# Performance work log

Hardware: AMD Instinct MI355X
Metric: run time of the kernel (lower is better)

The kernel has to match this reference:

```python
import jax, jax.numpy as jnp
import numpy as np
import math

RIEMANN_ZEROS_IM = (14.134725142, 21.022039639, 25.01085758, 30.424876126, 32.935061588,
    37.586178159, 40.918719012, 43.327073281, 48.005150881, 49.773832478, 52.970321478,
    56.446247697, 59.347044003, 60.831778525, 65.112544048, 67.079810529, 69.546401711,
    72.067157674, 75.704690699, 77.144840069, 79.33737502, 82.910380854, 84.735492981,
    87.425274613, 88.809111208, 92.491899271, 94.651344041, 95.870634228, 98.831194218,
    101.317851006, 103.72553804, 105.446623052)

D_MODEL = 1024
N_HEADS = 16
D_HEAD = D_MODEL // N_HEADS  # 64
N_PAIRS = D_HEAD // 2        # 32

# normalized inverse frequencies: gamma_n / gamma_1, inverted
_gamma = np.asarray(RIEMANN_ZEROS_IM[:N_PAIRS], dtype=np.float32)
INV_FREQ = jnp.asarray(1.0 / (_gamma / _gamma[0]))  # [n_pairs]


def _rotate(x, cos, sin):
    # x: [b,h,n,d_head]; cos/sin: [1,h,n,n_pairs]; interleaved pair rotation
    x1 = x[..., 0::2]
    x2 = x[..., 1::2]
    rx1 = x1 * cos - x2 * sin
    rx2 = x1 * sin + x2 * cos
    return jnp.stack([rx1, rx2], axis=-1).reshape(x.shape)


def setup_inputs() -> dict:
    key = jax.random.key(0)
    k1, k2, k3 = jax.random.split(key, 3)
    b, n = 4, 2048
    x = jax.random.normal(k1, (b, n, D_MODEL), dtype=jnp.float32)
    # torch Linear(d, 3d, bias=False): y = x @ W.T; we store W.T directly
    w_qkv = jax.random.normal(k2, (D_MODEL, 3 * D_MODEL), dtype=jnp.float32) / math.sqrt(D_MODEL)
    w_o = jax.random.normal(k3, (D_MODEL, D_MODEL), dtype=jnp.float32) / math.sqrt(D_MODEL)
    log_scale = jnp.zeros((N_HEADS,), dtype=jnp.float32)
    return {"x": x, "w_qkv": w_qkv, "w_o": w_o, "log_scale": log_scale}


def reference(x, w_qkv, w_o, log_scale):
    b, n, d = x.shape
    qkv = (x @ w_qkv).reshape(b, n, 3, N_HEADS, D_HEAD)
    q, k, v = qkv[:, :, 0], qkv[:, :, 1], qkv[:, :, 2]  # [b,n,h,dh]
    q = q.transpose(0, 2, 1, 3)  # [b,h,n,dh]
    k = k.transpose(0, 2, 1, 3)
    v = v.transpose(0, 2, 1, 3)

    scale = jnp.exp(log_scale)  # [h]
    pos = jnp.arange(n, dtype=jnp.float32)
    # theta: [1,h,n,n_pairs]
    theta = pos[None, None, :, None] * INV_FREQ[None, None, None, :] * scale[None, :, None, None]
    cos, sin = jnp.cos(theta), jnp.sin(theta)
    q = _rotate(q, cos, sin)
    k = _rotate(k, cos, sin)

    scores = jnp.einsum('bhqd,bhkd->bhqk', q, k) / math.sqrt(D_HEAD)
    causal = jnp.tril(jnp.ones((n, n), dtype=bool))
    scores = jnp.where(causal[None, None], scores, -jnp.inf)
    attn = jax.nn.softmax(scores, axis=-1)
    out = jnp.einsum('bhqk,bhkd->bhqd', attn, v)
    out = out.transpose(0, 2, 1, 3).reshape(b, n, d)
    return out @ w_o
```

## Files before the change

kernel.cpp:

```cpp
#include <hip/hip_runtime.h>
#include <hip/hip_bf16.h>

#define B_ 4
#define N_ 2048
#define DM 1024
#define NH 16
#define DH 64

typedef __attribute__((ext_vector_type(8))) __bf16 bf16x8;
typedef __attribute__((ext_vector_type(4))) float f32x4;
typedef __attribute__((ext_vector_type(4))) float float4v;
typedef __attribute__((ext_vector_type(4))) unsigned int uint4v;
typedef __attribute__((ext_vector_type(2))) unsigned int uint2v;
typedef __attribute__((ext_vector_type(4))) unsigned short ushort4v;

__device__ __forceinline__ float bf2f(unsigned short h) {
  union { unsigned int u; float f; } v; v.u = ((unsigned int)h) << 16; return v.f;
}
__device__ __forceinline__ unsigned short f2bf(float f) {
  __bf16 h = (__bf16)f;
  return __builtin_bit_cast(unsigned short, h);
}
__device__ __forceinline__ f32x4 mfma16(bf16x8 a, bf16x8 b, f32x4 c) {
  return __builtin_amdgcn_mfma_f32_16x16x32_bf16(a, b, c, 0, 0, 0);
}
__device__ __forceinline__ void gload_lds16(const void* g, void* l) {
  __builtin_amdgcn_global_load_lds(
      (const __attribute__((address_space(1))) unsigned int*)g,
      (__attribute__((address_space(3))) unsigned int*)l, 16, 0, 0);
}
__device__ __forceinline__ float fexp2(float x) {
  return __builtin_amdgcn_exp2f(x);
}

__constant__ float GAMMA_C[32] = {
  14.134725142f, 21.022039639f, 25.01085758f, 30.424876126f,
  32.935061588f, 37.586178159f, 40.918719012f, 43.327073281f,
  48.005150881f, 49.773832478f, 52.970321478f, 56.446247697f,
  59.347044003f, 60.831778525f, 65.112544048f, 67.079810529f,
  69.546401711f, 72.067157674f, 75.704690699f, 77.144840069f,
  79.33737502f,  82.910380854f, 84.735492981f, 87.425274613f,
  88.809111208f, 92.491899271f, 94.651344041f, 95.870634228f,
  98.831194218f, 101.317851006f, 103.72553804f, 105.446623052f
};

__global__ __launch_bounds__(256) void cast_f32_bf16(
    const float* __restrict__ in, unsigned short* __restrict__ out, int n4) {
  int i = blockIdx.x * 256 + threadIdx.x;
  if (i >= n4) return;
  float4v v = *(const float4v*)&in[(size_t)i * 4];
  ushort4v o;
  o[0] = f2bf(v[0]); o[1] = f2bf(v[1]); o[2] = f2bf(v[2]); o[3] = f2bf(v[3]);
  *(ushort4v*)&out[(size_t)i * 4] = o;
}

__global__ __launch_bounds__(256) void tcast(
    const float* __restrict__ in, unsigned short* __restrict__ out, int K, int N) {
  __shared__ float t[32][33];
  int n0 = blockIdx.x * 32, k0 = blockIdx.y * 32;
  int tx = threadIdx.x, ty = threadIdx.y;
#pragma unroll
  for (int j = 0; j < 4; ++j)
    t[ty + j * 8][tx] = in[(size_t)(k0 + ty + j * 8) * N + n0 + tx];
  __syncthreads();
#pragma unroll
  for (int j = 0; j < 4; ++j)
    out[(size_t)(n0 + ty + j * 8) * K + k0 + tx] = f2bf(t[tx][ty + j * 8]);
}

template <int OUTF32>
__global__ __launch_bounds__(256) void gemm_bt(
    const unsigned short* __restrict__ A, const unsigned short* __restrict__ BT,
    void* __restrict__ C, int M, int N, int K) {
  __shared__ unsigned short As[128 * 32];
  __shared__ unsigned short Bs[128 * 32];
  int tid = threadIdx.x;
  int lane = tid & 63, wid = tid >> 6;
  int wr = wid >> 1, wc = wid & 1;
  int lr = lane & 15, lg = lane >> 4;
  int bm = blockIdx.y * 128, bn = blockIdx.x * 128;
  int srow = lane >> 2, sch = lane & 3;
  f32x4 acc[4][4];
#pragma unroll
  for (int m = 0; m < 4; ++m)
#pragma unroll
    for (int n = 0; n < 4; ++n) acc[m][n] = (f32x4){0.f, 0.f, 0.f, 0.f};

  for (int k0 = 0; k0 < K; k0 += 32) {
    __syncthreads();
#pragma unroll
    for (int it = 0; it < 2; ++it) {
      int rbase = wid * 16 + it * 64;
      gload_lds16(&A[(size_t)(bm + rbase + srow) * K + k0 + sch * 8],
                  &As[rbase * 32]);
      gload_lds16(&BT[(size_t)(bn + rbase + srow) * K + k0 + sch * 8],
                  &Bs[rbase * 32]);
    }
    __syncthreads();
    bf16x8 af[4], bfr[4];
#pragma unroll
    for (int m = 0; m < 4; ++m)
      af[m] = *(const bf16x8*)&As[(wr * 64 + m * 16 + lr) * 32 + lg * 8];
#pragma unroll
    for (int n = 0; n < 4; ++n)
      bfr[n] = *(const bf16x8*)&Bs[(wc * 64 + n * 16 + lr) * 32 + lg * 8];
    __builtin_amdgcn_s_setprio(1);
#pragma unroll
    for (int m = 0; m < 4; ++m)
#pragma unroll
      for (int n = 0; n < 4; ++n)
        acc[m][n] = mfma16(af[m], bfr[n], acc[m][n]);
    __builtin_amdgcn_s_setprio(0);
  }
#pragma unroll
  for (int m = 0; m < 4; ++m)
#pragma unroll
    for (int n = 0; n < 4; ++n) {
      int row = bm + wr * 64 + m * 16 + lg * 4;
      int col = bn + wc * 64 + n * 16 + lr;
#pragma unroll
      for (int r = 0; r < 4; ++r) {
        if (OUTF32)
          ((float*)C)[(size_t)(row + r) * N + col] = acc[m][n][r];
        else
          ((unsigned short*)C)[(size_t)(row + r) * N + col] = f2bf(acc[m][n][r]);
      }
    }
}

__global__ __launch_bounds__(256) void rope_split(
    const unsigned short* __restrict__ qkv, const float* __restrict__ log_scale,
    unsigned short* __restrict__ Qr, unsigned short* __restrict__ Kr) {
  const float SC = 0.125f * 1.44269504089f;
  int t = blockIdx.x * 256 + threadIdx.x;
  int p = t & 31, h = (t >> 5) & 15, n = (t >> 9) & 2047, b = t >> 20;
  float invf = GAMMA_C[0] / GAMMA_C[p];
  float scale = __expf(log_scale[h]);
  float theta = ((float)n * invf) * scale;
  float sn, cs;
  sincosf(theta, &sn, &cs);
  size_t base = (size_t)(b * N_ + n) * (3 * DM) + h * DH + 2 * p;
  unsigned int qu = *(const unsigned int*)&qkv[base];
  unsigned int ku = *(const unsigned int*)&qkv[base + DM];
  float q1 = bf2f(qu & 0xffffu), q2 = bf2f(qu >> 16);
  float k1 = bf2f(ku & 0xffffu), k2 = bf2f(ku >> 16);
  unsigned int rq = (unsigned int)f2bf((q1 * cs - q2 * sn) * SC) |
                    ((unsigned int)f2bf((q1 * sn + q2 * cs) * SC) << 16);
  unsigned int rk = (unsigned int)f2bf(k1 * cs - k2 * sn) |
                    ((unsigned int)f2bf(k1 * sn + k2 * cs) << 16);
  size_t ob = (size_t)((b * NH + h) * N_ + n) * DH + 2 * p;
  *(unsigned int*)&Qr[ob] = rq;
  *(unsigned int*)&Kr[ob] = rk;
}

__global__ __launch_bounds__(256) void attn_fwd(
    const unsigned short* __restrict__ Q, const unsigned short* __restrict__ K,
    const unsigned short* __restrict__ qkv, unsigned short* __restrict__ AO) {
  int orig = blockIdx.x;
  int wg = (orig & 7) * 128 + (orig >> 3);
  int i = wg & 15;
  int qt = ((wg >> 5) & 1) ? (15 - i) : i;
  int bh = wg >> 4;
  int b = bh >> 4, h = bh & 15;
  int q0 = qt * 128;
  int tid = threadIdx.x;
  int lane = tid & 63, w = tid >> 6;
  int lr = lane & 15, lg = lane >> 4;

  const unsigned short* Qh = Q + (size_t)bh * N_ * DH;
  const unsigned short* Kh = K + (size_t)bh * N_ * DH;
  const unsigned short* Vq = qkv + (size_t)b * N_ * (3 * DM) + 2 * DM + h * DH;

  __shared__ unsigned short Ks[2][64 * 64];
  __shared__ unsigned short Vt[64 * 64];
  __shared__ unsigned int PsU[4][32][32];

  bf16x8 qf[2][2];
#pragma unroll
  for (int m = 0; m < 2; ++m)
#pragma unroll
    for (int dh = 0; dh < 2; ++dh)
      qf[m][dh] = *(const bf16x8*)
          &Qh[(size_t)(q0 + w * 32 + m * 16 + lr) * DH + dh * 32 + lg * 8];

  f32x4 oacc[2][4];
#pragma unroll
  for (int m = 0; m < 2; ++m)
#pragma unroll
    for (int nb = 0; nb < 4; ++nb) oacc[m][nb] = (f32x4){0.f, 0.f, 0.f, 0.f};
  float mst[2] = {-1e30f, -1e30f};
  float lst[2] = {0.f, 0.f};

  int wkend = q0 + w * 32 + 31;
  int ksup = q0 + 128;
  int vch = tid & 7, vk = tid >> 3;
  int swz = 4 * (lr & 7);

  auto KSTAGE = [&](int buf, int kk0) {
#pragma unroll
    for (int it = 0; it < 2; ++it) {
      int rbase = w * 8 + it * 32;
      int row = rbase + (lane >> 3);
      int sk = ((row & 7) ^ (row >> 3)) & 7;
      int ch = lane & 7;
      gload_lds16(&Kh[(size_t)(kk0 + row) * DH + ((ch ^ sk) * 8)],
                  &Ks[buf][rbase * 64]);
    }
  };
  auto VWRITE = [&](uint4v v0, uint4v v1) {
    const unsigned short* p0 = (const unsigned short*)&v0;
    const unsigned short* p1 = (const unsigned short*)&v1;
#pragma unroll
    for (int j = 0; j < 8; ++j) {
      int d = vch * 8 + j;
      int sv = (j ^ vch) & 7;
      Vt[d * 64 + (vk ^ (sv << 3))] = p0[j];
      Vt[d * 64 + ((vk + 32) ^ (sv << 3))] = p1[j];
    }
  };

  {
    uint4v v0 = *(const uint4v*)&Vq[(size_t)vk * (3 * DM) + vch * 8];
    uint4v v1 = *(const uint4v*)&Vq[(size_t)(vk + 32) * (3 * DM) + vch * 8];
    KSTAGE(0, 0);
    VWRITE(v0, v1);
    __syncthreads();
  }
  int cur = 0;

  for (int k0 = 0; k0 < ksup; k0 += 64) {
    bool hn = (k0 + 64 < ksup);
    uint4v nv0, nv1;
    if (hn) {
      nv0 = *(const uint4v*)&Vq[(size_t)(k0 + 64 + vk) * (3 * DM) + vch * 8];
      nv1 = *(const uint4v*)&Vq[(size_t)(k0 + 96 + vk) * (3 * DM) + vch * 8];
      KSTAGE(cur ^ 1, k0 + 64);
    }

    if (k0 <= wkend) {
      f32x4 s[2][4];
      __builtin_amdgcn_s_setprio(1);
#pragma unroll
      for (int nb = 0; nb < 4; ++nb) {
        int key = nb * 16 + lr;
        int sk = ((key & 7) ^ (key >> 3)) & 7;
        bf16x8 kf0 = *(const bf16x8*)&Ks[cur][key * 64 + ((lg ^ sk) * 8)];
        bf16x8 kf1 = *(const bf16x8*)&Ks[cur][key * 64 + (((4 + lg) ^ sk) * 8)];
#pragma unroll
        for (int m = 0; m < 2; ++m) {
          f32x4 z = (f32x4){0.f, 0.f, 0.f, 0.f};
          z = mfma16(kf0, qf[m][0], z);
          z = mfma16(kf1, qf[m][1], z);
          s[m][nb] = z;
        }
      }
      __builtin_amdgcn_s_setprio(0);

      float mx[2];
#pragma unroll
      for (int m = 0; m < 2; ++m) {
        int qm = q0 + w * 32 + m * 16;
        if (k0 + 63 > qm) {
          int q = qm + lr;
#pragma unroll
          for (int nb = 0; nb < 4; ++nb)
#pragma unroll
            for (int r = 0; r < 4; ++r)
              if (k0 + nb * 16 + lg * 4 + r > q) s[m][nb][r] = -1e30f;
        }
        float mx0 = fmaxf(fmaxf(s[m][0][0], s[m][0][1]),
                          fmaxf(s[m][0][2], s[m][0][3]));
        float mx1 = fmaxf(fmaxf(s[m][1][0], s[m][1][1]),
                          fmaxf(s[m][1][2], s[m][1][3]));
        float mx2 = fmaxf(fmaxf(s[m][2][0], s[m][2][1]),
                          fmaxf(s[m][2][2], s[m][2][3]));
        float mx3 = fmaxf(fmaxf(s[m][3][0], s[m][3][1]),
                          fmaxf(s[m][3][2], s[m][3][3]));
        float m01 = fmaxf(fmaxf(mx0, mx1), fmaxf(mx2, mx3));
        m01 = fmaxf(m01, __shfl_xor(m01, 16, 64));
        m01 = fmaxf(m01, __shfl_xor(m01, 32, 64));
        mx[m] = m01;
      }

      if (__any((mx[0] > mst[0] + 8.f) || (mx[1] > mst[1] + 8.f))) {
        float scs[2];
#pragma unroll
        for (int m = 0; m < 2; ++m) {
          float mnew = fmaxf(mst[m], mx[m]);
          float sc = fexp2(mst[m] - mnew);
          mst[m] = mnew;
          lst[m] *= sc;
          scs[m] = sc;
        }
#pragma unroll
        for (int m = 0; m < 2; ++m)
#pragma unroll
          for (int r = 0; r < 4; ++r) {
            float scr = __shfl(scs[m], lg * 4 + r, 64);
#pragma unroll
            for (int nb = 0; nb < 4; ++nb) oacc[m][nb][r] *= scr;
          }
      }

#pragma unroll
      for (int m = 0; m < 2; ++m) {
        float ps = 0.f;
        unsigned int pw[8];
#pragma unroll
        for (int nb = 0; nb < 4; ++nb)
#pragma unroll
          for (int rp = 0; rp < 2; ++rp) {
            float p0 = fexp2(s[m][nb][2 * rp] - mst[m]);
            float p1 = fexp2(s[m][nb][2 * rp + 1] - mst[m]);
            ps += p0 + p1;
            pw[nb * 2 + rp] =
                (unsigned int)f2bf(p0) | ((unsigned int)f2bf(p1) << 16);
          }
#pragma unroll
        for (int nb = 0; nb < 4; ++nb) {
          int c0 = (nb * 8 + lg * 2) ^ swz;
          *(uint2v*)&PsU[w][m * 16 + lr][c0] =
              (uint2v){pw[nb * 2], pw[nb * 2 + 1]};
        }
        ps += __shfl_xor(ps, 16, 64);
        ps += __shfl_xor(ps, 32, 64);
        lst[m] += ps;
      }
      asm volatile("s_waitcnt lgkmcnt(0)" ::: "memory");
      __builtin_amdgcn_sched_barrier(0);

      __builtin_amdgcn_s_setprio(1);
#pragma unroll
      for (int kh = 0; kh < 2; ++kh) {
        bf16x8 pf0 = *(const bf16x8*)&PsU[w][lr][(kh * 16 + lg * 4) ^ swz];
        bf16x8 pf1 = *(const bf16x8*)&PsU[w][16 + lr][(kh * 16 + lg * 4) ^ swz];
#pragma unroll
        for (int nb = 0; nb < 4; ++nb) {
          int d = nb * 16 + lr;
          int sv2 = ((d & 7) ^ (d >> 3)) & 7;
          bf16x8 vf = *(const bf16x8*)
              &Vt[d * 64 + ((kh * 32 + lg * 8) ^ (sv2 << 3))];
          oacc[0][nb] = mfma16(pf0, vf, oacc[0][nb]);
          oacc[1][nb] = mfma16(pf1, vf, oacc[1][nb]);
        }
      }
      __builtin_amdgcn_s_setprio(0);
    }

    __syncthreads();
    if (hn) {
      VWRITE(nv0, nv1);
      __syncthreads();
    }
    cur ^= 1;
  }

#pragma unroll
  for (int m = 0; m < 2; ++m) {
    float inv = 1.0f / lst[m];
#pragma unroll
    for (int r = 0; r < 4; ++r) {
      float invr = __shfl(inv, lg * 4 + r, 64);
      int q = q0 + w * 32 + m * 16 + lg * 4 + r;
#pragma unroll
      for (int nb = 0; nb < 4; ++nb) {
        float o = oacc[m][nb][r] * invr;
        AO[(size_t)(b * N_ + q) * DM + h * DH + nb * 16 + lr] = f2bf(o);
      }
    }
  }
}

extern "C" void kernel_launch(void* const* d_in, const int* in_sizes, int n_in,
                              void* d_out, int out_size, void* d_ws, size_t ws_size,
                              hipStream_t stream) {
  const float* x = (const float*)d_in[0];
  const float* w_qkv = (const float*)d_in[1];
  const float* w_o = (const float*)d_in[2];
  const float* log_scale = (const float*)d_in[3];
  float* out = (float*)d_out;

  char* ws = (char*)d_ws;
  unsigned short* xb  = (unsigned short*)(ws);
  unsigned short* ao  = xb;
  unsigned short* wqT = (unsigned short*)(ws + (16u << 20));
  unsigned short* woT = (unsigned short*)(ws + (22u << 20));
  unsigned short* qkv = (unsigned short*)(ws + (24u << 20));
  unsigned short* Qr  = (unsigned short*)(ws + (72u << 20));
  unsigned short* Kr  = (unsigned short*)(ws + (88u << 20));

  cast_f32_bf16<<<8192, 256, 0, stream>>>(x, xb, (B_ * N_ * DM) / 4);
  dim3 tb(32, 8);
  tcast<<<dim3(3 * DM / 32, DM / 32), tb, 0, stream>>>(w_qkv, wqT, DM, 3 * DM);
  tcast<<<dim3(DM / 32, DM / 32), tb, 0, stream>>>(w_o, woT, DM, DM);
  gemm_bt<0><<<dim3(3 * DM / 128, (B_ * N_) / 128), 256, 0, stream>>>(
      xb, wqT, qkv, B_ * N_, 3 * DM, DM);
  rope_split<<<(B_ * N_ * NH * 32) / 256, 256, 0, stream>>>(
      qkv, log_scale, Qr, Kr);
  attn_fwd<<<B_ * NH * (N_ / 128), 256, 0, stream>>>(Qr, Kr, qkv, ao);
  gemm_bt<1><<<dim3(DM / 128, (B_ * N_) / 128), 256, 0, stream>>>(
      ao, woT, out, B_ * N_, DM, DM);
}
```

Before: 246.6 us.

## Use 256x128 eight-wave GEMM for QKV and pair causal attention tiles per block

Adds a new gemm256 kernel for the QKV projection. It uses 256x128 output tiles, 512 threads, double-buffered LDS staging through dynamic shared memory, and a barrier-split compute schedule, replacing the 128x128 gemm_bt for that projection. The attention kernel now processes two query tiles per block (tile pi and 15-pi), which balances causal work and halves the grid to 512 blocks. Risks are lower occupancy from the 96KB of LDS and fewer waves in flight for attention, plus the extra barriers in the GEMM loop.

```diff
diff --git a/kernel.cpp b/kernel.cpp
--- a/kernel.cpp
+++ b/kernel.cpp
@@ -125,6 +125,126 @@
         else
           ((unsigned short*)C)[(size_t)(row + r) * N + col] = f2bf(acc[m][n][r]);
       }
+    }
+}
+
+__global__ __launch_bounds__(512) void gemm256(
+    const unsigned short* __restrict__ A, const unsigned short* __restrict__ BT,
+    unsigned short* __restrict__ C, int M, int N, int K) {
+  extern __shared__ unsigned short smem[];
+  unsigned short* Asb = smem;
+  unsigned short* Bsb = smem + 32768;
+  int tid = threadIdx.x;
+  int lane = tid & 63, w = tid >> 6;
+  int wr = w >> 2, wc = w & 3;
+  int lr = lane & 15, lg = lane >> 4;
+  int nbx = N >> 7;
+  int cpx = gridDim.x >> 3;
+  int orig = blockIdx.x;
+  int wg = (orig & 7) * cpx + (orig >> 3);
+  int bm = (wg / nbx) << 8, bn = (wg % nbx) << 7;
+  int srow = lane >> 3, sch = lane & 7;
+
+  f32x4 acc[8][2];
+#pragma unroll
+  for (int m = 0; m < 8; ++m)
+#pragma unroll
+    for (int n = 0; n < 2; ++n) acc[m][n] = (f32x4){0.f, 0.f, 0.f, 0.f};
+
+  auto STAGE = [&](int buf, int t) {
+    int k0 = t << 6;
+#pragma unroll
+    for (int it = 0; it < 4; ++it) {
+      int rbase = w * 32 + it * 8;
+      int row = rbase + srow;
+      int sk = row & 7;
+      gload_lds16(&A[(size_t)(bm + row) * K + k0 + ((sch ^ sk) * 8)],
+                  &Asb[buf * 16384 + rbase * 64]);
+    }
+#pragma unroll
+    for (int it = 0; it < 2; ++it) {
+      int rbase = w * 16 + it * 8;
+      int row = rbase + srow;
+      int sk = row & 7;
+      gload_lds16(&BT[(size_t)(bn + row) * K + k0 + ((sch ^ sk) * 8)],
+                  &Bsb[buf * 8192 + rbase * 64]);
+    }
+  };
+
+  int NT = K >> 6;
+  STAGE(0, 0);
+  STAGE(1, 1);
+  asm volatile("s_waitcnt vmcnt(6)" ::: "memory");
+  __builtin_amdgcn_s_barrier();
+
+  bf16x8 a[4][2], b[2][2];
+  int cur = 0;
+  for (int t = 0; t < NT; ++t) {
+    const unsigned short* Ab = &Asb[cur * 16384];
+    const unsigned short* Bb = &Bsb[cur * 8192];
+
+#define RD_A(half)                                                         \
+  {                                                                        \
+    _Pragma("unroll") for (int m4 = 0; m4 < 4; ++m4) {                     \
+      int ra = wr * 128 + (half) * 64 + m4 * 16 + lr;                      \
+      _Pragma("unroll") for (int kk = 0; kk < 2; ++kk)                     \
+          a[m4][kk] = *(const bf16x8*)                                     \
+              &Ab[ra * 64 + (((kk * 4 + lg) ^ (ra & 7)) * 8)];             \
+    }                                                                      \
+  }
+#define RD_B                                                               \
+  {                                                                        \
+    _Pragma("unroll") for (int n = 0; n < 2; ++n) {                        \
+      int rb = wc * 32 + n * 16 + lr;                                      \
+      _Pragma("unroll") for (int kk = 0; kk < 2; ++kk)                     \
+          b[n][kk] = *(const bf16x8*)                                      \
+              &Bb[rb * 64 + (((kk * 4 + lg) ^ (rb & 7)) * 8)];             \
+    }                                                                      \
+  }
+#define WAITL                                                              \
+  asm volatile("s_waitcnt lgkmcnt(0)" ::: "memory");                       \
+  __builtin_amdgcn_sched_barrier(0);
+#define MM(mh)                                                             \
+  __builtin_amdgcn_s_setprio(1);                                           \
+  _Pragma("unroll") for (int m4 = 0; m4 < 4; ++m4)                         \
+      _Pragma("unroll") for (int n = 0; n < 2; ++n)                        \
+          _Pragma("unroll") for (int kk = 0; kk < 2; ++kk)                 \
+              acc[(mh) * 4 + m4][n] =                                      \
+                  mfma16(a[m4][kk], b[n][kk], acc[(mh) * 4 + m4][n]);      \
+  __builtin_amdgcn_s_setprio(0);
+
+    RD_A(0); RD_B;
+    __builtin_amdgcn_s_barrier();
+    WAITL; MM(0);
+    __builtin_amdgcn_s_barrier();
+    RD_A(1);
+    __builtin_amdgcn_s_barrier();
+    WAITL; MM(1);
+    __builtin_amdgcn_s_barrier();
+
+    if (t + 2 < NT) {
+      STAGE(cur, t + 2);
+      asm volatile("s_waitcnt vmcnt(6)" ::: "memory");
+    } else if (t + 1 < NT) {
+      asm volatile("s_waitcnt vmcnt(0)" ::: "memory");
+    }
+    __builtin_amdgcn_s_barrier();
+    cur ^= 1;
+  }
+#undef RD_A
+#undef RD_B
+#undef WAITL
+#undef MM
+
+#pragma unroll
+  for (int m = 0; m < 8; ++m)
+#pragma unroll
+    for (int n = 0; n < 2; ++n) {
+      int row = bm + wr * 128 + m * 16 + lg * 4;
+      int col = bn + wc * 32 + n * 16 + lr;
+#pragma unroll
+      for (int r = 0; r < 4; ++r)
+        C[(size_t)(row + r) * N + col] = f2bf(acc[m][n][r]);
     }
 }
 
@@ -157,12 +277,10 @@
     const unsigned short* __restrict__ Q, const unsigned short* __restrict__ K,
     const unsigned short* __restrict__ qkv, unsigned short* __restrict__ AO) {
   int orig = blockIdx.x;
-  int wg = (orig & 7) * 128 + (orig >> 3);
-  int i = wg & 15;
-  int qt = ((wg >> 5) & 1) ? (15 - i) : i;
-  int bh = wg >> 4;
+  int wg = (orig & 7) * 64 + (orig >> 3);
+  int bh = wg >> 3;
+  int pi = wg & 7;
   int b = bh >> 4, h = bh & 15;
-  int q0 = qt * 128;
   int tid = threadIdx.x;
   int lane = tid & 63, w = tid >> 6;
   int lr = lane & 15, lg = lane >> 4;
@@ -175,24 +293,6 @@
   __shared__ unsigned short Vt[64 * 64];
   __shared__ unsigned int PsU[4][32][32];
 
-  bf16x8 qf[2][2];
-#pragma unroll
-  for (int m = 0; m < 2; ++m)
-#pragma unroll
-    for (int dh = 0; dh < 2; ++dh)
-      qf[m][dh] = *(const bf16x8*)
-          &Qh[(size_t)(q0 + w * 32 + m * 16 + lr) * DH + dh * 32 + lg * 8];
-
-  f32x4 oacc[2][4];
-#pragma unroll
-  for (int m = 0; m < 2; ++m)
-#pragma unroll
-    for (int nb = 0; nb < 4; ++nb) oacc[m][nb] = (f32x4){0.f, 0.f, 0.f, 0.f};
-  float mst[2] = {-1e30f, -1e30f};
-  float lst[2] = {0.f, 0.f};
-
-  int wkend = q0 + w * 32 + 31;
-  int ksup = q0 + 128;
   int vch = tid & 7, vk = tid >> 3;
   int swz = 4 * (lr & 7);
 
@@ -219,153 +319,177 @@
     }
   };
 
-  {
-    uint4v v0 = *(const uint4v*)&Vq[(size_t)vk * (3 * DM) + vch * 8];
-    uint4v v1 = *(const uint4v*)&Vq[(size_t)(vk + 32) * (3 * DM) + vch * 8];
-    KSTAGE(0, 0);
-    VWRITE(v0, v1);
-    __syncthreads();
-  }
-  int cur = 0;
-
-  for (int k0 = 0; k0 < ksup; k0 += 64) {
-    bool hn = (k0 + 64 < ksup);
-    uint4v nv0, nv1;
-    if (hn) {
-      nv0 = *(const uint4v*)&Vq[(size_t)(k0 + 64 + vk) * (3 * DM) + vch * 8];
-      nv1 = *(const uint4v*)&Vq[(size_t)(k0 + 96 + vk) * (3 * DM) + vch * 8];
-      KSTAGE(cur ^ 1, k0 + 64);
-    }
-
-    if (k0 <= wkend) {
-      f32x4 s[2][4];
-      __builtin_amdgcn_s_setprio(1);
-#pragma unroll
-      for (int nb = 0; nb < 4; ++nb) {
-        int key = nb * 16 + lr;
-        int sk = ((key & 7) ^ (key >> 3)) & 7;
-        bf16x8 kf0 = *(const bf16x8*)&Ks[cur][key * 64 + ((lg ^ sk) * 8)];
-        bf16x8 kf1 = *(const bf16x8*)&Ks[cur][key * 64 + (((4 + lg) ^ sk) * 8)];
+  for (int half = 0; half < 2; ++half) {
+    int qt = half ? (15 - pi) : pi;
+    int q0 = qt * 128;
+
+    bf16x8 qf[2][2];
+#pragma unroll
+    for (int m = 0; m < 2; ++m)
+#pragma unroll
+      for (int dh = 0; dh < 2; ++dh)
+        qf[m][dh] = *(const bf16x8*)
+            &Qh[(size_t)(q0 + w * 32 + m * 16 + lr) * DH + dh * 32 + lg * 8];
+
+    f32x4 oacc[2][4];
+#pragma unroll
+    for (int m = 0; m < 2; ++m)
+#pragma unroll
+      for (int nb = 0; nb < 4; ++nb) oacc[m][nb] = (f32x4){0.f, 0.f, 0.f, 0.f};
+    float mst[2] = {-1e30f, -1e30f};
+    float lst[2] = {0.f, 0.f};
+
+    int wkend = q0 + w * 32 + 31;
+    int ksup = q0 + 128;
+
+    {
+      uint4v v0 = *(const uint4v*)&Vq[(size_t)vk * (3 * DM) + vch * 8];
+      uint4v v1 = *(const uint4v*)&Vq[(size_t)(vk + 32) * (3 * DM) + vch * 8];
+      KSTAGE(0, 0);
+      VWRITE(v0, v1);
+      __syncthreads();
+    }
+    int cur = 0;
+
+    for (int k0 = 0; k0 < ksup; k0 += 64) {
+      bool hn = (k0 + 64 < ksup);
+      uint4v nv0, nv1;
+      if (hn) {
+        nv0 = *(const uint4v*)&Vq[(size_t)(k0 + 64 + vk) * (3 * DM) + vch * 8];
+        nv1 = *(const uint4v*)&Vq[(size_t)(k0 + 96 + vk) * (3 * DM) + vch * 8];
+        KSTAGE(cur ^ 1, k0 + 64);
+      }
+
+      if (k0 <= wkend) {
+        f32x4 s[2][4];
+        __builtin_amdgcn_s_setprio(1);
+#pragma unroll
+        for (int nb = 0; nb < 4; ++nb) {
+          int key = nb * 16 + lr;
+          int sk = ((key & 7) ^ (key >> 3)) & 7;
+          bf16x8 kf0 = *(const bf16x8*)&Ks[cur][key * 64 + ((lg ^ sk) * 8)];
+          bf16x8 kf1 = *(const bf16x8*)&Ks[cur][key * 64 + (((4 + lg) ^ sk) * 8)];
+#pragma unroll
+          for (int m = 0; m < 2; ++m) {
+            f32x4 z = (f32x4){0.f, 0.f, 0.f, 0.f};
+            z = mfma16(kf0, qf[m][0], z);
+            z = mfma16(kf1, qf[m][1], z);
+            s[m][nb] = z;
+          }
+        }
+        __builtin_amdgcn_s_setprio(0);
+
+        float mx[2];
 #pragma unroll
         for (int m = 0; m < 2; ++m) {
-          f32x4 z = (f32x4){0.f, 0.f, 0.f, 0.f};
-          z = mfma16(kf0, qf[m][0], z);
-          z = mfma16(kf1, qf[m][1], z);
-          s[m][nb] = z;
+          int qm = q0 + w * 32 + m * 16;
+          if (k0 + 63 > qm) {
+            int q = qm + lr;
+#pragma unroll
+            for (int nb = 0; nb < 4; ++nb)
+#pragma unroll
+              for (int r = 0; r < 4; ++r)
+                if (k0 + nb * 16 + lg * 4 + r > q) s[m][nb][r] = -1e30f;
+          }
+          float mx0 = fmaxf(fmaxf(s[m][0][0], s[m][0][1]),
+                            fmaxf(s[m][0][2], s[m][0][3]));
+          float mx1 = fmaxf(fmaxf(s[m][1][0], s[m][1][1]),
+                            fmaxf(s[m][1][2], s[m][1][3]));
+          float mx2 = fmaxf(fmaxf(s[m][2][0], s[m][2][1]),
+                            fmaxf(s[m][2][2], s[m][2][3]));
+          float mx3 = fmaxf(fmaxf(s[m][3][0], s[m][3][1]),
+                            fmaxf(s[m][3][2], s[m][3][3]));
+          float m01 = fmaxf(fmaxf(mx0, mx1), fmaxf(mx2, mx3));
+          m01 = fmaxf(m01, __shfl_xor(m01, 16, 64));
+          m01 = fmaxf(m01, __shfl_xor(m01, 32, 64));
+          mx[m] = m01;
         }
+
+        if (__any((mx[0] > mst[0] + 8.f) || (mx[1] > mst[1] + 8.f))) {
+          float scs[2];
+#pragma unroll
+          for (int m = 0; m < 2; ++m) {
+            float mnew = fmaxf(mst[m], mx[m]);
+            float sc = fexp2(mst[m] - mnew);
+            mst[m] = mnew;
+            lst[m] *= sc;
+            scs[m] = sc;
+          }
+#pragma unroll
+          for (int m = 0; m < 2; ++m)
+#pragma unroll
+            for (int r = 0; r < 4; ++r) {
+              float scr = __shfl(scs[m], lg * 4 + r, 64);
+#pragma unroll
+              for (int nb = 0; nb < 4; ++nb) oacc[m][nb][r] *= scr;
+            }
+        }
+
+#pragma unroll
+        for (int m = 0; m < 2; ++m) {
+          float ps = 0.f;
+          unsigned int pw[8];
+#pragma unroll
+          for (int nb = 0; nb < 4; ++nb)
+#pragma unroll
+            for (int rp = 0; rp < 2; ++rp) {
+              float p0 = fexp2(s[m][nb][2 * rp] - mst[m]);
+              float p1 = fexp2(s[m][nb][2 * rp + 1] - mst[m]);
+              ps += p0 + p1;
+              pw[nb * 2 + rp] =
+                  (unsigned int)f2bf(p0) | ((unsigned int)f2bf(p1) << 16);
+            }
+#pragma unroll
+          for (int nb = 0; nb < 4; ++nb) {
+            int c0 = (nb * 8 + lg * 2) ^ swz;
+            *(uint2v*)&PsU[w][m * 16 + lr][c0] =
+                (uint2v){pw[nb * 2], pw[nb * 2 + 1]};
+          }
+          ps += __shfl_xor(ps, 16, 64);
+          ps += __shfl_xor(ps, 32, 64);
+          lst[m] += ps;
+        }
+        asm volatile("s_waitcnt lgkmcnt(0)" ::: "memory");
+        __builtin_amdgcn_sched_barrier(0);
+
+        __builtin_amdgcn_s_setprio(1);
+#pragma unroll
+        for (int kh = 0; kh < 2; ++kh) {
+          bf16x8 pf0 = *(const bf16x8*)&PsU[w][lr][(kh * 16 + lg * 4) ^ swz];
+          bf16x8 pf1 = *(const bf16x8*)&PsU[w][16 + lr][(kh * 16 + lg * 4) ^ swz];
+#pragma unroll
+          for (int nb = 0; nb < 4; ++nb) {
+            int d = nb * 16 + lr;
+            int sv2 = ((d & 7) ^ (d >> 3)) & 7;
+            bf16x8 vf = *(const bf16x8*)
+                &Vt[d * 64 + ((kh * 32 + lg * 8) ^ (sv2 << 3))];
+            oacc[0][nb] = mfma16(pf0, vf, oacc[0][nb]);
+            oacc[1][nb] = mfma16(pf1, vf, oacc[1][nb]);
+          }
+        }
+        __builtin_amdgcn_s_setprio(0);
       }
-      __builtin_amdgcn_s_setprio(0);
-
-      float mx[2];
-#pragma unroll
-      for (int m = 0; m < 2; ++m) {
-        int qm = q0 + w * 32 + m * 16;
-        if (k0 + 63 > qm) {
-          int q = qm + lr;
-#pragma unroll
-          for (int nb = 0; nb < 4; ++nb)
-#pragma unroll
-            for (int r = 0; r < 4; ++r)
-              if (k0 + nb * 16 + lg * 4 + r > q) s[m][nb][r] = -1e30f;
+
+      __syncthreads();
+      if (hn) {
+        VWRITE(nv0, nv1);
+        __syncthreads();
+      }
+      cur ^= 1;
+    }
+
+#pragma unroll
+    for (int m = 0; m < 2; ++m) {
+      float inv = 1.0f / lst[m];
+#pragma unroll
+      for (int r = 0; r < 4; ++r) {
+        float invr = __shfl(inv, lg * 4 + r, 64);
+        int q = q0 + w * 32 + m * 16 + lg * 4 + r;
+#pragma unroll
+        for (int nb = 0; nb < 4; ++nb) {
+          float o = oacc[m][nb][r] * invr;
+          AO[(size_t)(b * N_ + q) * DM + h * DH + nb * 16 + lr] = f2bf(o);
         }
-        float mx0 = fmaxf(fmaxf(s[m][0][0], s[m][0][1]),
-                          fmaxf(s[m][0][2], s[m][0][3]));
-        float mx1 = fmaxf(fmaxf(s[m][1][0], s[m][1][1]),
-                          fmaxf(s[m][1][2], s[m][1][3]));
-        float mx2 = fmaxf(fmaxf(s[m][2][0], s[m][2][1]),
-                          fmaxf(s[m][2][2], s[m][2][3]));
-        float mx3 = fmaxf(fmaxf(s[m][3][0], s[m][3][1]),
-                          fmaxf(s[m][3][2], s[m][3][3]));
-        float m01 = fmaxf(fmaxf(mx0, mx1), fmaxf(mx2, mx3));
-        m01 = fmaxf(m01, __shfl_xor(m01, 16, 64));
-        m01 = fmaxf(m01, __shfl_xor(m01, 32, 64));
-        mx[m] = m01;
-      }
-
-      if (__any((mx[0] > mst[0] + 8.f) || (mx[1] > mst[1] + 8.f))) {
-        float scs[2];
-#pragma unroll
-        for (int m = 0; m < 2; ++m) {
-          float mnew = fmaxf(mst[m], mx[m]);
-          float sc = fexp2(mst[m] - mnew);
-          mst[m] = mnew;
-          lst[m] *= sc;
-          scs[m] = sc;
-        }
-#pragma unroll
-        for (int m = 0; m < 2; ++m)
-#pragma unroll
-          for (int r = 0; r < 4; ++r) {
-            float scr = __shfl(scs[m], lg * 4 + r, 64);
-#pragma unroll
-            for (int nb = 0; nb < 4; ++nb) oacc[m][nb][r] *= scr;
-          }
-      }
-
-#pragma unroll
-      for (int m = 0; m < 2; ++m) {
-        float ps = 0.f;
-        unsigned int pw[8];
-#pragma unroll
-        for (int nb = 0; nb < 4; ++nb)
-#pragma unroll
-          for (int rp = 0; rp < 2; ++rp) {
-            float p0 = fexp2(s[m][nb][2 * rp] - mst[m]);
-            float p1 = fexp2(s[m][nb][2 * rp + 1] - mst[m]);
-            ps += p0 + p1;
-            pw[nb * 2 + rp] =
-                (unsigned int)f2bf(p0) | ((unsigned int)f2bf(p1) << 16);
-          }
-#pragma unroll
-        for (int nb = 0; nb < 4; ++nb) {
-          int c0 = (nb * 8 + lg * 2) ^ swz;
-          *(uint2v*)&PsU[w][m * 16 + lr][c0] =
-              (uint2v){pw[nb * 2], pw[nb * 2 + 1]};
-        }
-        ps += __shfl_xor(ps, 16, 64);
-        ps += __shfl_xor(ps, 32, 64);
-        lst[m] += ps;
-      }
-      asm volatile("s_waitcnt lgkmcnt(0)" ::: "memory");
-      __builtin_amdgcn_sched_barrier(0);
-
-      __builtin_amdgcn_s_setprio(1);
-#pragma unroll
-      for (int kh = 0; kh < 2; ++kh) {
-        bf16x8 pf0 = *(const bf16x8*)&PsU[w][lr][(kh * 16 + lg * 4) ^ swz];
-        bf16x8 pf1 = *(const bf16x8*)&PsU[w][16 + lr][(kh * 16 + lg * 4) ^ swz];
-#pragma unroll
-        for (int nb = 0; nb < 4; ++nb) {
-          int d = nb * 16 + lr;
-          int sv2 = ((d & 7) ^ (d >> 3)) & 7;
-          bf16x8 vf = *(const bf16x8*)
-              &Vt[d * 64 + ((kh * 32 + lg * 8) ^ (sv2 << 3))];
-          oacc[0][nb] = mfma16(pf0, vf, oacc[0][nb]);
-          oacc[1][nb] = mfma16(pf1, vf, oacc[1][nb]);
-        }
-      }
-      __builtin_amdgcn_s_setprio(0);
-    }
-
-    __syncthreads();
-    if (hn) {
-      VWRITE(nv0, nv1);
-      __syncthreads();
-    }
-    cur ^= 1;
-  }
-
-#pragma unroll
-  for (int m = 0; m < 2; ++m) {
-    float inv = 1.0f / lst[m];
-#pragma unroll
-    for (int r = 0; r < 4; ++r) {
-      float invr = __shfl(inv, lg * 4 + r, 64);
-      int q = q0 + w * 32 + m * 16 + lg * 4 + r;
-#pragma unroll
-      for (int nb = 0; nb < 4; ++nb) {
-        float o = oacc[m][nb][r] * invr;
-        AO[(size_t)(b * N_ + q) * DM + h * DH + nb * 16 + lr] = f2bf(o);
       }
     }
   }
@@ -389,15 +513,18 @@
   unsigned short* Qr  = (unsigned short*)(ws + (72u << 20));
   unsigned short* Kr  = (unsigned short*)(ws + (88u << 20));
 
+  hipFuncSetAttribute((const void*)gemm256,
+                      hipFuncAttributeMaxDynamicSharedMemorySize, 98304);
+
   cast_f32_bf16<<<8192, 256, 0, stream>>>(x, xb, (B_ * N_ * DM) / 4);
   dim3 tb(32, 8);
   tcast<<<dim3(3 * DM / 32, DM / 32), tb, 0, stream>>>(w_qkv, wqT, DM, 3 * DM);
   tcast<<<dim3(DM / 32, DM / 32), tb, 0, stream>>>(w_o, woT, DM, DM);
-  gemm_bt<0><<<dim3(3 * DM / 128, (B_ * N_) / 128), 256, 0, stream>>>(
+  gemm256<<<(B_ * N_ / 256) * (3 * DM / 128), 512, 98304, stream>>>(
       xb, wqT, qkv, B_ * N_, 3 * DM, DM);
   rope_split<<<(B_ * N_ * NH * 32) / 256, 256, 0, stream>>>(
       qkv, log_scale, Qr, Kr);
-  attn_fwd<<<B_ * NH * (N_ / 128), 256, 0, stream>>>(Qr, Kr, qkv, ao);
+  attn_fwd<<<B_ * NH * 8, 256, 0, stream>>>(Qr, Kr, qkv, ao);
   gemm_bt<1><<<dim3(DM / 128, (B_ * N_) / 128), 256, 0, stream>>>(
       ao, woT, out, B_ * N_, DM, DM);
 }
```

Measured after the change: 265.7 us. +7.7%, slower.
